# Kernel tuning notes

Measured on AMD Instinct MI355X. Metric: run time of the kernel, lower is better.

## Reference

```python
import jax, jax.numpy as jnp
import numpy as np

B, N, C, H = 2, 2048, 1024, 16
D = C // H  # head_dim = 64


def setup_inputs() -> dict:
    key = jax.random.key(0)
    ks = jax.random.split(key, 5)
    s = 1.0 / np.sqrt(C)
    return {
        "q": jax.random.normal(ks[0], (B, N, C), dtype=jnp.float32),
        "W_qkv": jax.random.normal(ks[1], (C, 3 * C), dtype=jnp.float32) * s,
        "b_qkv": jnp.zeros((3 * C,), dtype=jnp.float32),
        "W_proj": jax.random.normal(ks[2], (C, C), dtype=jnp.float32) * s,
        "b_proj": jnp.zeros((C,), dtype=jnp.float32),
    }


def reference(q, W_qkv, b_qkv, W_proj, b_proj):
    # Self-attention: k = v = q. Full 3C projection (as in the torch code).
    qkv = q @ W_qkv + b_qkv  # [B, N, 3C]
    qh = qkv[:, :, :C].reshape(B, N, H, D)
    kh = qkv[:, :, C:2 * C].reshape(B, N, H, D)
    vh = qkv[:, :, 2 * C:].reshape(B, N, H, D)
    scale = D ** -0.5
    # [B, H, N, N] attention logits
    attn = jnp.einsum("bnhd,bmhd->bhnm", qh, kh) * scale
    attn = jax.nn.softmax(attn, axis=-1)
    out = jnp.einsum("bhnm,bmhd->bnhd", attn, vh).reshape(B, N, C)
    return out @ W_proj + b_proj
```

## Files before the change

### kernel.cpp

```cpp
#include <hip/hip_runtime.h>
#include <stdint.h>

typedef __bf16 bf16_t;
typedef __bf16 bf16x8 __attribute__((ext_vector_type(8)));
typedef __bf16 bf16x4 __attribute__((ext_vector_type(4)));
typedef float f32x4 __attribute__((ext_vector_type(4)));

#define L2E 1.44269504088896340736f
#define QSCALE (0.125f * L2E)

__device__ __forceinline__ void gload16(const bf16_t* g, bf16_t* l) {
  __builtin_amdgcn_global_load_lds(
      (const __attribute__((address_space(1))) void*)g,
      (__attribute__((address_space(3))) void*)l, 16, 0, 0);
}

__global__ __launch_bounds__(256) void cast_q_kernel(const float* __restrict__ in,
                                                     bf16_t* __restrict__ out) {
  int i = blockIdx.x * 256 + threadIdx.x;
  float4 v = reinterpret_cast<const float4*>(in)[i];
  bf16x4 o;
  o[0] = (bf16_t)v.x; o[1] = (bf16_t)v.y; o[2] = (bf16_t)v.z; o[3] = (bf16_t)v.w;
  reinterpret_cast<bf16x4*>(out)[i] = o;
}

__global__ __launch_bounds__(256) void transpose_cast_kernel(const float* __restrict__ in,
                                                             bf16_t* __restrict__ out,
                                                             int K, int N) {
  __shared__ float tile[64][65];
  int k0 = blockIdx.y * 64, n0 = blockIdx.x * 64;
  int t = threadIdx.x;
  int r = t >> 4, c4 = (t & 15) * 4;
#pragma unroll
  for (int rr = 0; rr < 4; rr++) {
    int row = r + rr * 16;
    float4 v = *reinterpret_cast<const float4*>(&in[(size_t)(k0 + row) * N + n0 + c4]);
    tile[row][c4 + 0] = v.x; tile[row][c4 + 1] = v.y;
    tile[row][c4 + 2] = v.z; tile[row][c4 + 3] = v.w;
  }
  __syncthreads();
#pragma unroll
  for (int rr = 0; rr < 4; rr++) {
    int nr = r + rr * 16;
    bf16x4 o;
#pragma unroll
    for (int i = 0; i < 4; i++) o[i] = (bf16_t)tile[c4 + i][nr];
    *reinterpret_cast<bf16x4*>(&out[(size_t)(n0 + nr) * K + k0 + c4]) = o;
  }
}

template <int MODE, int BM>
__global__ __launch_bounds__(256) void gemm_kernel(const bf16_t* __restrict__ A,
                                                   const bf16_t* __restrict__ Bt,
                                                   const float* __restrict__ bias,
                                                   void* __restrict__ out,
                                                   bf16_t* __restrict__ vT,
                                                   int K, int gm, int gn, int ldo) {
  constexpr int ACH = BM / 8;
  constexpr int NCH = ACH + 16;
  constexpr int CPW = NCH / 4;
  constexpr int IR = BM / 32;
  constexpr int SMEM = (MODE == 0) ? 17408 : (BM * 64 + 8192);
  __shared__ __align__(16) bf16_t smem[SMEM];
  bf16_t* At = smem;
  bf16_t* Bts = smem + BM * 64;
  const int t = threadIdx.x, lane = t & 63, w = t >> 6;
  const int g = lane >> 4, q = lane & 15;
  const int bid = blockIdx.x, x = bid & 7, r = bid >> 3;
  const int qm = gm >> 2, qn = gn >> 1;
  const int lm = r % qm, ln = r / qm;
  const int m0 = ((x & 3) * qm + lm) * BM, n0 = ((x >> 2) * qn + ln) * 128;
  const int wm = (w >> 1) * (BM / 2), wn = (w & 1) * 64;

  const bf16_t* srcp[CPW]; int dsto[CPW];
#pragma unroll
  for (int i = 0; i < CPW; i++) {
    int cI = i * 4 + w;
    bool isA = cI < ACH;
    int row = (isA ? cI : cI - ACH) * 8 + (lane >> 3);
    int p = (lane & 7) ^ (row & 7);
    srcp[i] = (isA ? A + (size_t)(m0 + row) * K : Bt + (size_t)(n0 + row) * K) + p * 8;
    dsto[i] = (isA ? cI * 512 : BM * 64 + (cI - ACH) * 512) - (size_t)lane * 8;
    dsto[i] = (isA ? cI * 512 : BM * 64 + (cI - ACH) * 512);
  }

  f32x4 acc[IR][4];
#pragma unroll
  for (int i = 0; i < IR; i++)
#pragma unroll
    for (int j = 0; j < 4; j++) acc[i][j] = (f32x4){0.f, 0.f, 0.f, 0.f};

  for (int k0 = 0; k0 < K; k0 += 64) {
    __syncthreads();
#pragma unroll
    for (int i = 0; i < CPW; i++) gload16(srcp[i] + k0, &smem[dsto[i]]);
    __syncthreads();
#pragma unroll
    for (int dc = 0; dc < 2; dc++) {
      bf16x8 am[IR], bn[4];
#pragma unroll
      for (int i = 0; i < IR; i++) {
        int ra = wm + 16 * i + q;
        am[i] = *reinterpret_cast<const bf16x8*>(&At[ra * 64 + ((dc * 32 + g * 8) ^ ((ra & 7) * 8))]);
      }
#pragma unroll
      for (int j = 0; j < 4; j++) {
        int rb = wn + 16 * j + q;
        bn[j] = *reinterpret_cast<const bf16x8*>(&Bts[rb * 64 + ((dc * 32 + g * 8) ^ ((rb & 7) * 8))]);
      }
      __builtin_amdgcn_s_setprio(1);
#pragma unroll
      for (int i = 0; i < IR; i++)
#pragma unroll
        for (int j = 0; j < 4; j++)
          acc[i][j] = __builtin_amdgcn_mfma_f32_16x16x32_bf16(am[i], bn[j], acc[i][j], 0, 0, 0);
      __builtin_amdgcn_s_setprio(0);
    }
  }

  if (MODE == 0 && n0 >= 2048) {
    __syncthreads();
    bf16_t* TT = smem;
#pragma unroll
    for (int i = 0; i < IR; i++)
#pragma unroll
      for (int j = 0; j < 4; j++)
#pragma unroll
        for (int rr = 0; rr < 4; rr++) {
          int ch = wn + 16 * j + q;
          int tok = wm + 16 * i + 4 * g + rr;
          float v = acc[i][j][rr] + bias[n0 + ch];
          TT[ch * 136 + (((tok >> 3) ^ (ch & 7)) * 8) + (tok & 7)] = (bf16_t)v;
        }
    __syncthreads();
    const int bb = m0 >> 11;
    const int t0 = m0 & 2047;
#pragma unroll
    for (int it = 0; it < 8; it++) {
      int ch = it * 16 + w * 4 + (lane >> 4);
      int ck = lane & 15;
      uint4 val = *reinterpret_cast<const uint4*>(&TT[ch * 136 + ((ck ^ (ch & 7)) * 8)]);
      int vch = (n0 - 2048) + ch;
      bf16_t* dst = vT + ((size_t)(bb * 16 + (vch >> 6)) * 64 + (vch & 63)) * 2048 + t0 + ck * 8;
      *reinterpret_cast<uint4*>(dst) = val;
    }
  } else {
#pragma unroll
    for (int i = 0; i < IR; i++)
#pragma unroll
      for (int j = 0; j < 4; j++)
#pragma unroll
        for (int rr = 0; rr < 4; rr++) {
          int row = m0 + wm + 16 * i + 4 * g + rr;
          int col = n0 + wn + 16 * j + q;
          float v = acc[i][j][rr] + bias[col];
          if (MODE == 0) {
            if (col < 1024) v *= QSCALE;
            ((bf16_t*)out)[(size_t)row * ldo + col] = (bf16_t)v;
          } else {
            ((float*)out)[(size_t)row * ldo + col] = v;
          }
        }
  }
}

__global__ __launch_bounds__(256) void attn_kernel(const bf16_t* __restrict__ qk,
                                                   const bf16_t* __restrict__ vT,
                                                   bf16_t* __restrict__ aout) {
  __shared__ __align__(16) bf16_t sK[2][4096];
  __shared__ __align__(16) bf16_t sV[2][4096];
  __shared__ __align__(16) bf16_t sP[4][2048];

  const int t = threadIdx.x, lane = t & 63, w = t >> 6;
  const int g = lane >> 4, q = lane & 15;
  const int bid = blockIdx.x, xr = bid >> 3;
  const int bh = (bid & 7) * 4 + (xr >> 4);
  const int b = bh >> 4, h = bh & 15;
  const int q0 = (xr & 15) * 128 + w * 16;
  const bf16_t* qk_b = qk + (size_t)b * 2048 * 2048;
  const bf16_t* vT_h = vT + (size_t)bh * 64 * 2048;
  bf16_t* Pw = sP[w];

  const bf16_t* srcK[2]; const bf16_t* srcV[2]; int dsto[2];
#pragma unroll
  for (int i = 0; i < 2; i++) {
    int gI = (w * 2 + i) * 64 + lane;
    int row = gI >> 3, p = (gI & 7) ^ (row & 7);
    srcK[i] = qk_b + (size_t)row * 2048 + 1024 + h * 64 + p * 8;
    srcV[i] = vT_h + (size_t)row * 2048 + p * 8;
    dsto[i] = (w * 2 + i) * 512;
  }

  bf16x8 bq[2][2];
#pragma unroll
  for (int s = 0; s < 2; s++) {
    const bf16_t* qr = qk_b + (size_t)(q0 + s * 64 + q) * 2048 + h * 64;
    bq[s][0] = *reinterpret_cast<const bf16x8*>(qr + g * 8);
    bq[s][1] = *reinterpret_cast<const bf16x8*>(qr + 32 + g * 8);
  }

  bf16x8 ones;
#pragma unroll
  for (int i = 0; i < 8; i++) ones[i] = (bf16_t)1.0f;

  f32x4 oacc[2][4];
#pragma unroll
  for (int s = 0; s < 2; s++)
#pragma unroll
    for (int c = 0; c < 4; c++) oacc[s][c] = (f32x4){0.f, 0.f, 0.f, 0.f};
  f32x4 lacc[2];
  lacc[0] = (f32x4){0.f, 0.f, 0.f, 0.f};
  lacc[1] = (f32x4){0.f, 0.f, 0.f, 0.f};

#pragma unroll
  for (int i = 0; i < 2; i++) {
    gload16(srcK[i], &sK[0][dsto[i]]);
    gload16(srcV[i], &sV[0][dsto[i]]);
  }
  __syncthreads();

  for (int tt = 0; tt < 32; tt++) {
    const int cur = tt & 1;
    if (tt + 1 < 32) {
      size_t koffK = (size_t)(tt + 1) * 64 * 2048;
      size_t koffV = (size_t)(tt + 1) * 64;
#pragma unroll
      for (int i = 0; i < 2; i++) {
        gload16(srcK[i] + koffK, &sK[cur ^ 1][dsto[i]]);
        gload16(srcV[i] + koffV, &sV[cur ^ 1][dsto[i]]);
      }
    }

    const bf16_t* Kc = sK[cur];
    bf16x8 kf[4][2];
#pragma unroll
    for (int c = 0; c < 4; c++) {
      int row = 16 * c + q, sw = (q & 7) * 8;
      kf[c][0] = *reinterpret_cast<const bf16x8*>(&Kc[row * 64 + ((g * 8) ^ sw)]);
      kf[c][1] = *reinterpret_cast<const bf16x8*>(&Kc[row * 64 + ((32 + g * 8) ^ sw)]);
    }
    f32x4 s0[4], s1[4];
    __builtin_amdgcn_s_setprio(1);
#pragma unroll
    for (int c = 0; c < 4; c++) {
      f32x4 z = (f32x4){0.f, 0.f, 0.f, 0.f};
      z = __builtin_amdgcn_mfma_f32_16x16x32_bf16(kf[c][0], bq[0][0], z, 0, 0, 0);
      s0[c] = __builtin_amdgcn_mfma_f32_16x16x32_bf16(kf[c][1], bq[0][1], z, 0, 0, 0);
      f32x4 z1 = (f32x4){0.f, 0.f, 0.f, 0.f};
      z1 = __builtin_amdgcn_mfma_f32_16x16x32_bf16(kf[c][0], bq[1][0], z1, 0, 0, 0);
      s1[c] = __builtin_amdgcn_mfma_f32_16x16x32_bf16(kf[c][1], bq[1][1], z1, 0, 0, 0);
    }
    __builtin_amdgcn_s_setprio(0);

#pragma unroll
    for (int c = 0; c < 4; c++) {
      bf16x4 pk0, pk1;
#pragma unroll
      for (int rr = 0; rr < 4; rr++) {
        pk0[rr] = (bf16_t)exp2f(s0[c][rr]);
        pk1[rr] = (bf16_t)exp2f(s1[c][rr]);
      }
      int off = q * 64 + (((2 * c + (g >> 1)) ^ (q & 7)) * 8) + (g & 1) * 4;
      *reinterpret_cast<bf16x4*>(&Pw[off]) = pk0;
      *reinterpret_cast<bf16x4*>(&Pw[1024 + off]) = pk1;
    }

    const bf16_t* Vc = sV[cur];
    __builtin_amdgcn_s_setprio(1);
#pragma unroll
    for (int kc = 0; kc < 2; kc++) {
      int poff = q * 64 + (((kc * 4 + g) ^ (q & 7)) * 8);
      bf16x8 pb0 = *reinterpret_cast<const bf16x8*>(&Pw[poff]);
      bf16x8 pb1 = *reinterpret_cast<const bf16x8*>(&Pw[1024 + poff]);
      lacc[0] = __builtin_amdgcn_mfma_f32_16x16x32_bf16(ones, pb0, lacc[0], 0, 0, 0);
      lacc[1] = __builtin_amdgcn_mfma_f32_16x16x32_bf16(ones, pb1, lacc[1], 0, 0, 0);
#pragma unroll
      for (int c = 0; c < 4; c++) {
        int row = 16 * c + q;
        bf16x8 va = *reinterpret_cast<const bf16x8*>(
            &Vc[row * 64 + (((kc * 4 + g) ^ (q & 7)) * 8)]);
        oacc[0][c] = __builtin_amdgcn_mfma_f32_16x16x32_bf16(va, pb0, oacc[0][c], 0, 0, 0);
        oacc[1][c] = __builtin_amdgcn_mfma_f32_16x16x32_bf16(va, pb1, oacc[1][c], 0, 0, 0);
      }
    }
    __builtin_amdgcn_s_setprio(0);

    __syncthreads();
  }

#pragma unroll
  for (int s = 0; s < 2; s++) {
    float inv = 1.0f / lacc[s][0];
    bf16_t* orow = aout + (size_t)(b * 2048 + q0 + s * 64 + q) * 1024 + h * 64;
#pragma unroll
    for (int c = 0; c < 4; c++) {
      bf16x4 ov;
#pragma unroll
      for (int rr = 0; rr < 4; rr++) ov[rr] = (bf16_t)(oacc[s][c][rr] * inv);
      *reinterpret_cast<bf16x4*>(orow + c * 16 + g * 4) = ov;
    }
  }
}

extern "C" void kernel_launch(void* const* d_in, const int* in_sizes, int n_in,
                              void* d_out, int out_size, void* d_ws, size_t ws_size,
                              hipStream_t stream) {
  const float* q     = (const float*)d_in[0];
  const float* Wqkv  = (const float*)d_in[1];
  const float* bqkv  = (const float*)d_in[2];
  const float* Wproj = (const float*)d_in[3];
  const float* bproj = (const float*)d_in[4];
  float* out = (float*)d_out;

  char* ws = (char*)d_ws;
  bf16_t* q_bf    = (bf16_t*)(ws);
  bf16_t* wqkv_t  = (bf16_t*)(ws + 8388608);
  bf16_t* wproj_t = (bf16_t*)(ws + 14680064);
  bf16_t* qk      = (bf16_t*)(ws + 16777216);
  bf16_t* vT      = (bf16_t*)(ws + 33554432);
  bf16_t* aout    = q_bf;

  cast_q_kernel<<<4096, 256, 0, stream>>>(q, q_bf);
  transpose_cast_kernel<<<dim3(48, 16), 256, 0, stream>>>(Wqkv, wqkv_t, 1024, 3072);
  transpose_cast_kernel<<<dim3(16, 16), 256, 0, stream>>>(Wproj, wproj_t, 1024, 1024);
  gemm_kernel<0, 128><<<768, 256, 0, stream>>>(q_bf, wqkv_t, bqkv, qk, vT, 1024, 32, 24, 2048);
  attn_kernel<<<512, 256, 0, stream>>>(qk, vT, aout);
  gemm_kernel<1, 64><<<512, 256, 0, stream>>>(aout, wproj_t, bproj, out, nullptr, 1024, 64, 8, 1024);
}
```

Before: 145.6 us.

## Fuse prep kernels, halve attention block size, use raw v_exp, drop setprio

Merges the q cast and both weight transpose-casts into one prep kernel to save launches. The attention kernel now runs 1024 blocks of 2 waves, each wave owning 32 query rows, instead of 512 blocks of 4 waves; this doubles K/V tile loads per block relative to its queries but raises block count and occupancy. exp2f is replaced with an inline v_exp_f32, and the s_setprio hints are removed from both the GEMM and attention loops. K fragment loads are interleaved with their MFMAs.

```diff
diff --git a/kernel.cpp b/kernel.cpp
--- a/kernel.cpp
+++ b/kernel.cpp
@@ -15,21 +15,36 @@
       (__attribute__((address_space(3))) void*)l, 16, 0, 0);
 }
 
-__global__ __launch_bounds__(256) void cast_q_kernel(const float* __restrict__ in,
-                                                     bf16_t* __restrict__ out) {
-  int i = blockIdx.x * 256 + threadIdx.x;
-  float4 v = reinterpret_cast<const float4*>(in)[i];
-  bf16x4 o;
-  o[0] = (bf16_t)v.x; o[1] = (bf16_t)v.y; o[2] = (bf16_t)v.z; o[3] = (bf16_t)v.w;
-  reinterpret_cast<bf16x4*>(out)[i] = o;
-}
-
-__global__ __launch_bounds__(256) void transpose_cast_kernel(const float* __restrict__ in,
-                                                             bf16_t* __restrict__ out,
-                                                             int K, int N) {
+__device__ __forceinline__ float fexp2(float x) {
+  float r;
+  asm("v_exp_f32 %0, %1" : "=v"(r) : "v"(x));
+  return r;
+}
+
+__global__ __launch_bounds__(256) void prep_kernel(const float* __restrict__ qin,
+                                                   bf16_t* __restrict__ qbf,
+                                                   const float* __restrict__ wqkv,
+                                                   bf16_t* __restrict__ wqkv_t,
+                                                   const float* __restrict__ wproj,
+                                                   bf16_t* __restrict__ wproj_t) {
   __shared__ float tile[64][65];
-  int k0 = blockIdx.y * 64, n0 = blockIdx.x * 64;
-  int t = threadIdx.x;
+  const int bid = blockIdx.x, t = threadIdx.x;
+  if (bid < 4096) {
+    int i = bid * 256 + t;
+    float4 v = reinterpret_cast<const float4*>(qin)[i];
+    bf16x4 o;
+    o[0] = (bf16_t)v.x; o[1] = (bf16_t)v.y; o[2] = (bf16_t)v.z; o[3] = (bf16_t)v.w;
+    reinterpret_cast<bf16x4*>(qbf)[i] = o;
+    return;
+  }
+  const float* in; bf16_t* out; int N, bx, by;
+  if (bid < 4864) {
+    int bb = bid - 4096; in = wqkv; out = wqkv_t; N = 3072; bx = bb % 48; by = bb / 48;
+  } else {
+    int bb = bid - 4864; in = wproj; out = wproj_t; N = 1024; bx = bb % 16; by = bb / 16;
+  }
+  const int K = 1024;
+  int k0 = by * 64, n0 = bx * 64;
   int r = t >> 4, c4 = (t & 15) * 4;
 #pragma unroll
   for (int rr = 0; rr < 4; rr++) {
@@ -80,7 +95,6 @@
     int row = (isA ? cI : cI - ACH) * 8 + (lane >> 3);
     int p = (lane & 7) ^ (row & 7);
     srcp[i] = (isA ? A + (size_t)(m0 + row) * K : Bt + (size_t)(n0 + row) * K) + p * 8;
-    dsto[i] = (isA ? cI * 512 : BM * 64 + (cI - ACH) * 512) - (size_t)lane * 8;
     dsto[i] = (isA ? cI * 512 : BM * 64 + (cI - ACH) * 512);
   }
 
@@ -108,13 +122,11 @@
         int rb = wn + 16 * j + q;
         bn[j] = *reinterpret_cast<const bf16x8*>(&Bts[rb * 64 + ((dc * 32 + g * 8) ^ ((rb & 7) * 8))]);
       }
-      __builtin_amdgcn_s_setprio(1);
 #pragma unroll
       for (int i = 0; i < IR; i++)
 #pragma unroll
         for (int j = 0; j < 4; j++)
           acc[i][j] = __builtin_amdgcn_mfma_f32_16x16x32_bf16(am[i], bn[j], acc[i][j], 0, 0, 0);
-      __builtin_amdgcn_s_setprio(0);
     }
   }
 
@@ -164,37 +176,37 @@
   }
 }
 
-__global__ __launch_bounds__(256) void attn_kernel(const bf16_t* __restrict__ qk,
+__global__ __launch_bounds__(128) void attn_kernel(const bf16_t* __restrict__ qk,
                                                    const bf16_t* __restrict__ vT,
                                                    bf16_t* __restrict__ aout) {
   __shared__ __align__(16) bf16_t sK[2][4096];
   __shared__ __align__(16) bf16_t sV[2][4096];
-  __shared__ __align__(16) bf16_t sP[4][2048];
+  __shared__ __align__(16) bf16_t sP[2][2048];
 
   const int t = threadIdx.x, lane = t & 63, w = t >> 6;
   const int g = lane >> 4, q = lane & 15;
   const int bid = blockIdx.x, xr = bid >> 3;
-  const int bh = (bid & 7) * 4 + (xr >> 4);
+  const int bh = (bid & 7) * 4 + (xr >> 5);
   const int b = bh >> 4, h = bh & 15;
-  const int q0 = (xr & 15) * 128 + w * 16;
+  const int q0 = (xr & 31) * 64 + w * 32;
   const bf16_t* qk_b = qk + (size_t)b * 2048 * 2048;
   const bf16_t* vT_h = vT + (size_t)bh * 64 * 2048;
   bf16_t* Pw = sP[w];
 
-  const bf16_t* srcK[2]; const bf16_t* srcV[2]; int dsto[2];
-#pragma unroll
-  for (int i = 0; i < 2; i++) {
-    int gI = (w * 2 + i) * 64 + lane;
+  const bf16_t* srcK[4]; const bf16_t* srcV[4]; int dsto[4];
+#pragma unroll
+  for (int i = 0; i < 4; i++) {
+    int gI = (w * 4 + i) * 64 + lane;
     int row = gI >> 3, p = (gI & 7) ^ (row & 7);
     srcK[i] = qk_b + (size_t)row * 2048 + 1024 + h * 64 + p * 8;
     srcV[i] = vT_h + (size_t)row * 2048 + p * 8;
-    dsto[i] = (w * 2 + i) * 512;
+    dsto[i] = (w * 4 + i) * 512;
   }
 
   bf16x8 bq[2][2];
 #pragma unroll
   for (int s = 0; s < 2; s++) {
-    const bf16_t* qr = qk_b + (size_t)(q0 + s * 64 + q) * 2048 + h * 64;
+    const bf16_t* qr = qk_b + (size_t)(q0 + s * 16 + q) * 2048 + h * 64;
     bq[s][0] = *reinterpret_cast<const bf16x8*>(qr + g * 8);
     bq[s][1] = *reinterpret_cast<const bf16x8*>(qr + 32 + g * 8);
   }
@@ -208,12 +220,11 @@
   for (int s = 0; s < 2; s++)
 #pragma unroll
     for (int c = 0; c < 4; c++) oacc[s][c] = (f32x4){0.f, 0.f, 0.f, 0.f};
-  f32x4 lacc[2];
-  lacc[0] = (f32x4){0.f, 0.f, 0.f, 0.f};
-  lacc[1] = (f32x4){0.f, 0.f, 0.f, 0.f};
-
-#pragma unroll
-  for (int i = 0; i < 2; i++) {
+  f32x4 lacc0 = (f32x4){0.f, 0.f, 0.f, 0.f};
+  f32x4 lacc1 = (f32x4){0.f, 0.f, 0.f, 0.f};
+
+#pragma unroll
+  for (int i = 0; i < 4; i++) {
     gload16(srcK[i], &sK[0][dsto[i]]);
     gload16(srcV[i], &sV[0][dsto[i]]);
   }
@@ -225,40 +236,34 @@
       size_t koffK = (size_t)(tt + 1) * 64 * 2048;
       size_t koffV = (size_t)(tt + 1) * 64;
 #pragma unroll
-      for (int i = 0; i < 2; i++) {
+      for (int i = 0; i < 4; i++) {
         gload16(srcK[i] + koffK, &sK[cur ^ 1][dsto[i]]);
         gload16(srcV[i] + koffV, &sV[cur ^ 1][dsto[i]]);
       }
     }
 
     const bf16_t* Kc = sK[cur];
-    bf16x8 kf[4][2];
+    f32x4 s0[4], s1[4];
 #pragma unroll
     for (int c = 0; c < 4; c++) {
       int row = 16 * c + q, sw = (q & 7) * 8;
-      kf[c][0] = *reinterpret_cast<const bf16x8*>(&Kc[row * 64 + ((g * 8) ^ sw)]);
-      kf[c][1] = *reinterpret_cast<const bf16x8*>(&Kc[row * 64 + ((32 + g * 8) ^ sw)]);
-    }
-    f32x4 s0[4], s1[4];
-    __builtin_amdgcn_s_setprio(1);
-#pragma unroll
-    for (int c = 0; c < 4; c++) {
-      f32x4 z = (f32x4){0.f, 0.f, 0.f, 0.f};
-      z = __builtin_amdgcn_mfma_f32_16x16x32_bf16(kf[c][0], bq[0][0], z, 0, 0, 0);
-      s0[c] = __builtin_amdgcn_mfma_f32_16x16x32_bf16(kf[c][1], bq[0][1], z, 0, 0, 0);
+      bf16x8 ka0 = *reinterpret_cast<const bf16x8*>(&Kc[row * 64 + ((g * 8) ^ sw)]);
+      bf16x8 ka1 = *reinterpret_cast<const bf16x8*>(&Kc[row * 64 + ((32 + g * 8) ^ sw)]);
+      f32x4 z0 = (f32x4){0.f, 0.f, 0.f, 0.f};
+      z0 = __builtin_amdgcn_mfma_f32_16x16x32_bf16(ka0, bq[0][0], z0, 0, 0, 0);
+      s0[c] = __builtin_amdgcn_mfma_f32_16x16x32_bf16(ka1, bq[0][1], z0, 0, 0, 0);
       f32x4 z1 = (f32x4){0.f, 0.f, 0.f, 0.f};
-      z1 = __builtin_amdgcn_mfma_f32_16x16x32_bf16(kf[c][0], bq[1][0], z1, 0, 0, 0);
-      s1[c] = __builtin_amdgcn_mfma_f32_16x16x32_bf16(kf[c][1], bq[1][1], z1, 0, 0, 0);
-    }
-    __builtin_amdgcn_s_setprio(0);
+      z1 = __builtin_amdgcn_mfma_f32_16x16x32_bf16(ka0, bq[1][0], z1, 0, 0, 0);
+      s1[c] = __builtin_amdgcn_mfma_f32_16x16x32_bf16(ka1, bq[1][1], z1, 0, 0, 0);
+    }
 
 #pragma unroll
     for (int c = 0; c < 4; c++) {
       bf16x4 pk0, pk1;
 #pragma unroll
       for (int rr = 0; rr < 4; rr++) {
-        pk0[rr] = (bf16_t)exp2f(s0[c][rr]);
-        pk1[rr] = (bf16_t)exp2f(s1[c][rr]);
+        pk0[rr] = (bf16_t)fexp2(s0[c][rr]);
+        pk1[rr] = (bf16_t)fexp2(s1[c][rr]);
       }
       int off = q * 64 + (((2 * c + (g >> 1)) ^ (q & 7)) * 8) + (g & 1) * 4;
       *reinterpret_cast<bf16x4*>(&Pw[off]) = pk0;
@@ -266,14 +271,13 @@
     }
 
     const bf16_t* Vc = sV[cur];
-    __builtin_amdgcn_s_setprio(1);
 #pragma unroll
     for (int kc = 0; kc < 2; kc++) {
       int poff = q * 64 + (((kc * 4 + g) ^ (q & 7)) * 8);
       bf16x8 pb0 = *reinterpret_cast<const bf16x8*>(&Pw[poff]);
       bf16x8 pb1 = *reinterpret_cast<const bf16x8*>(&Pw[1024 + poff]);
-      lacc[0] = __builtin_amdgcn_mfma_f32_16x16x32_bf16(ones, pb0, lacc[0], 0, 0, 0);
-      lacc[1] = __builtin_amdgcn_mfma_f32_16x16x32_bf16(ones, pb1, lacc[1], 0, 0, 0);
+      lacc0 = __builtin_amdgcn_mfma_f32_16x16x32_bf16(ones, pb0, lacc0, 0, 0, 0);
+      lacc1 = __builtin_amdgcn_mfma_f32_16x16x32_bf16(ones, pb1, lacc1, 0, 0, 0);
 #pragma unroll
       for (int c = 0; c < 4; c++) {
         int row = 16 * c + q;
@@ -283,15 +287,14 @@
         oacc[1][c] = __builtin_amdgcn_mfma_f32_16x16x32_bf16(va, pb1, oacc[1][c], 0, 0, 0);
       }
     }
-    __builtin_amdgcn_s_setprio(0);
 
     __syncthreads();
   }
 
 #pragma unroll
   for (int s = 0; s < 2; s++) {
-    float inv = 1.0f / lacc[s][0];
-    bf16_t* orow = aout + (size_t)(b * 2048 + q0 + s * 64 + q) * 1024 + h * 64;
+    float inv = 1.0f / (s ? lacc1[0] : lacc0[0]);
+    bf16_t* orow = aout + (size_t)(b * 2048 + q0 + s * 16 + q) * 1024 + h * 64;
 #pragma unroll
     for (int c = 0; c < 4; c++) {
       bf16x4 ov;
@@ -320,10 +323,8 @@
   bf16_t* vT      = (bf16_t*)(ws + 33554432);
   bf16_t* aout    = q_bf;
 
-  cast_q_kernel<<<4096, 256, 0, stream>>>(q, q_bf);
-  transpose_cast_kernel<<<dim3(48, 16), 256, 0, stream>>>(Wqkv, wqkv_t, 1024, 3072);
-  transpose_cast_kernel<<<dim3(16, 16), 256, 0, stream>>>(Wproj, wproj_t, 1024, 1024);
+  prep_kernel<<<5120, 256, 0, stream>>>(q, q_bf, Wqkv, wqkv_t, Wproj, wproj_t);
   gemm_kernel<0, 128><<<768, 256, 0, stream>>>(q_bf, wqkv_t, bqkv, qk, vT, 1024, 32, 24, 2048);
-  attn_kernel<<<512, 256, 0, stream>>>(qk, vT, aout);
+  attn_kernel<<<1024, 128, 0, stream>>>(qk, vT, aout);
   gemm_kernel<1, 64><<<512, 256, 0, stream>>>(aout, wproj_t, bproj, out, nullptr, 1024, 64, 8, 1024);
 }
```

Result: faster. 133.4 us (-8.4%).
